# Performance work log

Hardware: AMD Instinct MI355X
Metric: run time of the kernel (lower is better)

Reference implementation:

```python
import jax, jax.numpy as jnp
import numpy as np

N_NODES = 50000
N_EDGES = 800000
D = 128        # in_channels == out_channels
EDGE_DIM = 32
EPS = 0.0      # GINEConv default eps


def setup_inputs() -> dict:
    key = jax.random.key(0)
    ks = jax.random.split(key, 12)
    s = lambda d: 1.0 / np.sqrt(d)
    inp = {
        "x": jax.random.normal(ks[0], (N_NODES, D), jnp.float32),
        "edge_index": jax.random.randint(ks[1], (2, N_EDGES), 0, N_NODES, jnp.int64),
        "edge_attr": jax.random.normal(ks[2], (N_EDGES, EDGE_DIM), jnp.float32),
        "importance": jax.random.uniform(ks[3], (N_NODES, 1), jnp.float32),
        # GINEConv edge lin: Linear(edge_dim, in_channels)
        "We": jax.random.uniform(ks[4], (EDGE_DIM, D), jnp.float32, -s(EDGE_DIM), s(EDGE_DIM)),
        "be": jax.random.uniform(ks[5], (D,), jnp.float32, -s(EDGE_DIM), s(EDGE_DIM)),
        # GINEConv nn: Linear(in_channels, out_channels)
        "Wc": jax.random.uniform(ks[6], (D, D), jnp.float32, -s(D), s(D)),
        "bc": jax.random.uniform(ks[7], (D,), jnp.float32, -s(D), s(D)),
        # importance_gate: Linear(out_channels + 1, out_channels)
        "Wg": jax.random.uniform(ks[8], (D + 1, D), jnp.float32, -s(D + 1), s(D + 1)),
        "bg": jax.random.uniform(ks[9], (D,), jnp.float32, -s(D + 1), s(D + 1)),
        # importance_propagation: Linear(out_channels, 1)
        "Wp": jax.random.uniform(ks[10], (D, 1), jnp.float32, -s(D), s(D)),
        "bp": jax.random.uniform(ks[11], (1,), jnp.float32, -s(D), s(D)),
    }
    return inp


def reference(x, edge_index, edge_attr, importance, We, be, Wc, bc, Wg, bg, Wp, bp):
    src, dst = edge_index[0], edge_index[1]
    # GINEConv: messages = relu(x_j + lin(edge_attr)), aggregated by sum at dst
    e = edge_attr @ We + be                      # [E, D]
    msg = jax.nn.relu(x[src] + e)                # [E, D] gather + fused add/relu
    agg = jax.ops.segment_sum(msg, dst, num_segments=N_NODES)  # [N, D] scatter-add
    conv_out = ((1.0 + EPS) * x + agg) @ Wc + bc  # [N, D]
    # importance gating + residual
    gate_in = jnp.concatenate([conv_out, importance], axis=-1)  # [N, D+1]
    gate = jax.nn.sigmoid(gate_in @ Wg + bg)
    out = gate * conv_out + (1.0 - gate) * x
    propagated_importance = out @ Wp + bp        # [N, 1]
    return (out, propagated_importance)
```

## Files before the change

kernel.cpp:

```cpp
#include <hip/hip_runtime.h>

#define NN 50000
#define NE 800000
#define DD 128
#define ED 32
#define NB 196

typedef short  bf16x8 __attribute__((ext_vector_type(8)));
typedef float  f32x4  __attribute__((ext_vector_type(4)));
typedef float  f32x16 __attribute__((ext_vector_type(16)));

__device__ __forceinline__ float4 ld4(const float* p) {
    return *reinterpret_cast<const float4*>(p);
}
__device__ __forceinline__ short f2bf(float f) {
    unsigned u = __float_as_uint(f);
    u += 0x7fffu + ((u >> 16) & 1u);
    return (short)(u >> 16);
}
__device__ __forceinline__ int sniff64(const int* ei) {
    return ((ei[1] | ei[3] | ei[5] | ei[7]) == 0) ? 1 : 0;
}

__global__ __launch_bounds__(256)
void k_setup(const float* __restrict__ x, const int* __restrict__ ei,
             const float* __restrict__ We, unsigned int* __restrict__ xb,
             int* __restrict__ counts, unsigned short* __restrict__ Bft)
{
    const int tid = threadIdx.x;
    if (blockIdx.x < 6250) {
        const int t = blockIdx.x * 256 + tid;
        if (t >= NN * 32) return;
        const int n = t >> 5, c = t & 31;
        const float* xr = x + (size_t)n * DD + c;
        const unsigned b0 = (unsigned short)f2bf(xr[0]);
        const unsigned b1 = (unsigned short)f2bf(xr[32]);
        const unsigned b2 = (unsigned short)f2bf(xr[64]);
        const unsigned b3 = (unsigned short)f2bf(xr[96]);
        xb[(size_t)n * 64 + c * 2]     = b0 | (b1 << 16);
        xb[(size_t)n * 64 + c * 2 + 1] = b2 | (b3 << 16);
    } else if (blockIdx.x < 8298) {
        const int is64 = sniff64(ei);
        const int2* ei2 = (const int2*)ei;
        for (int e = (blockIdx.x - 6250) * 256 + tid; e < NE; e += 2048 * 256) {
            const int dst = is64 ? ei2[NE + e].x : ei[NE + e];
            atomicAdd(&counts[dst], 1);
        }
    } else if (tid < 64) {
        const int col = tid & 31, h = tid >> 5;
#pragma unroll
        for (int bb = 0; bb < 4; ++bb)
#pragma unroll
            for (int s = 0; s < 2; ++s)
#pragma unroll
                for (int i = 0; i < 8; ++i)
                    Bft[tid * 64 + (bb * 2 + s) * 8 + i] =
                        (unsigned short)f2bf(We[(s * 16 + h * 8 + i) * DD + bb * 32 + col]);
    }
}

__global__ __launch_bounds__(256)
void k_bsum(const int* __restrict__ counts, int* __restrict__ bsum) {
    const int i = blockIdx.x * 256 + threadIdx.x;
    int c = (i < NN) ? counts[i] : 0;
#pragma unroll
    for (int off = 32; off; off >>= 1) c += __shfl_xor(c, off, 64);
    __shared__ int ws4[4];
    if ((threadIdx.x & 63) == 0) ws4[threadIdx.x >> 6] = c;
    __syncthreads();
    if (threadIdx.x == 0) bsum[blockIdx.x] = ws4[0] + ws4[1] + ws4[2] + ws4[3];
}

__global__ __launch_bounds__(256)
void k_scanb(const int* __restrict__ bsum, int* __restrict__ bexcl) {
    const int tid = threadIdx.x, lane = tid & 63, w = tid >> 6;
    const int v = (tid < NB) ? bsum[tid] : 0;
    int s = v;
#pragma unroll
    for (int off = 1; off < 64; off <<= 1) {
        const int t = __shfl_up(s, off, 64);
        if (lane >= off) s += t;
    }
    __shared__ int wsum[4], wexcl[4];
    if (lane == 63) wsum[w] = s;
    __syncthreads();
    if (tid == 0) {
        int r = 0;
#pragma unroll
        for (int k = 0; k < 4; ++k) { wexcl[k] = r; r += wsum[k]; }
    }
    __syncthreads();
    if (tid < NB) bexcl[tid] = wexcl[w] + s - v;
}

__global__ __launch_bounds__(256)
void k_rowptr(const int* __restrict__ counts, const int* __restrict__ bexcl,
              int* __restrict__ cursor) {
    const int tid = threadIdx.x, lane = tid & 63, w = tid >> 6;
    const int i = blockIdx.x * 256 + tid;
    const int c = (i < NN) ? counts[i] : 0;
    int s = c;
#pragma unroll
    for (int off = 1; off < 64; off <<= 1) {
        const int t = __shfl_up(s, off, 64);
        if (lane >= off) s += t;
    }
    __shared__ int wsum[4], wexcl[4];
    if (lane == 63) wsum[w] = s;
    __syncthreads();
    if (tid == 0) {
        int r = 0;
#pragma unroll
        for (int k = 0; k < 4; ++k) { wexcl[k] = r; r += wsum[k]; }
    }
    __syncthreads();
    if (i < NN) cursor[i] = bexcl[blockIdx.x] + wexcl[w] + s - c;
}

__global__ __launch_bounds__(256)
void k_scatter2(const int* __restrict__ ei, int* __restrict__ cursor,
                const float* __restrict__ ea, int2* __restrict__ sdat,
                unsigned int* __restrict__ eb)
{
    const int tid = threadIdx.x;
    const int e0  = blockIdx.x * 128;
    if (tid < 128) {
        const int is64 = sniff64(ei);
        const int2* ei2 = (const int2*)ei;
        const int e   = e0 + tid;
        const int src = is64 ? ei2[e].x : ei[e];
        const int dst = is64 ? ei2[NE + e].x : ei[NE + e];
        const int pos = atomicAdd(&cursor[dst], 1);
        sdat[pos] = make_int2(src | (dst << 16), e);
    }
#pragma unroll
    for (int it = 0; it < 8; ++it) {
        const int idx = it * 256 + tid;
        const float2 v = *reinterpret_cast<const float2*>(
                             ea + (size_t)e0 * ED + idx * 2);
        const unsigned lo = (unsigned short)f2bf(v.x);
        const unsigned hi = (unsigned short)f2bf(v.y);
        eb[(size_t)e0 * 16 + idx] = lo | (hi << 16);
    }
}

__device__ __forceinline__ void agg_epilogue(f32x16 (&C)[4], const float beb[4],
                                             int dstv, int lane, int col, int h,
                                             float* __restrict__ agg)
{
#pragma unroll
    for (int bb = 0; bb < 4; ++bb)
#pragma unroll
        for (int reg = 0; reg < 16; ++reg)
            C[bb][reg] = fmaxf(C[bb][reg] + beb[bb], 0.0f);

    const int  prv  = __shfl(dstv, (lane == 0) ? 0 : lane - 1, 64);
    const bool flag = (lane < 32) && ((col == 0) || (dstv != prv));
    unsigned rem = (unsigned)(__ballot(flag) & 0xFFFFFFFFull);

    while (rem) {
        const int ms = __ffs((int)rem) - 1;
        rem &= rem - 1;
        const int hi = rem ? (__ffs((int)rem) - 1) : 32;
        const int d  = __shfl(dstv, ms, 64);

        float v0 = 0.f, v1 = 0.f, v2 = 0.f, v3 = 0.f;
#pragma unroll
        for (int reg = 0; reg < 16; ++reg) {
            const int E = (reg & 3) + 8 * (reg >> 2) + 4 * h;
            const float mk = (E >= ms && E < hi) ? 1.0f : 0.0f;
            v0 = fmaf(mk, C[0][reg], v0);
            v1 = fmaf(mk, C[1][reg], v1);
            v2 = fmaf(mk, C[2][reg], v2);
            v3 = fmaf(mk, C[3][reg], v3);
        }
        v0 += __shfl_xor(v0, 32, 64);
        v1 += __shfl_xor(v1, 32, 64);
        v2 += __shfl_xor(v2, 32, 64);
        v3 += __shfl_xor(v3, 32, 64);

        float* ar = agg + (size_t)d * DD + h * 64 + col;
        unsafeAtomicAdd(ar,      h ? v2 : v0);
        unsafeAtomicAdd(ar + 32, h ? v3 : v1);
    }
}

__global__ __launch_bounds__(256, 2)
void k_aggE(const unsigned int* __restrict__ xb, const unsigned int* __restrict__ eb,
            const unsigned short* __restrict__ Bft, const float* __restrict__ be,
            const int2* __restrict__ sdat, float* __restrict__ agg)
{
    const int lane = threadIdx.x & 63;
    const int col  = lane & 31;
    const int h    = lane >> 5;
    const int wid  = (blockIdx.x << 2) | (threadIdx.x >> 6);
    const int c0   = wid * 2, c1 = wid * 2 + 1;

    bf16x8 Bf[4][2];
    {
        const bf16x8* bp_ = reinterpret_cast<const bf16x8*>(Bft + lane * 64);
#pragma unroll
        for (int bb = 0; bb < 4; ++bb) {
            Bf[bb][0] = bp_[bb * 2];
            Bf[bb][1] = bp_[bb * 2 + 1];
        }
    }
    float beb[4];
#pragma unroll
    for (int bb = 0; bb < 4; ++bb) beb[bb] = be[bb * 32 + col];

    const int2 dv0 = sdat[(size_t)c0 * 32 + col];
    const int2 dv1 = sdat[(size_t)c1 * 32 + col];

    const unsigned int* ebr0 = eb + (size_t)dv0.y * 16;
    const unsigned int* ebr1 = eb + (size_t)dv1.y * 16;
    const bf16x8 A00 = *reinterpret_cast<const bf16x8*>(ebr0 + h * 4);
    const bf16x8 A01 = *reinterpret_cast<const bf16x8*>(ebr0 + 8 + h * 4);
    const bf16x8 A10 = *reinterpret_cast<const bf16x8*>(ebr1 + h * 4);
    const bf16x8 A11 = *reinterpret_cast<const bf16x8*>(ebr1 + 8 + h * 4);

    uint2 w0[16];
#pragma unroll
    for (int reg = 0; reg < 16; ++reg) {
        const int E   = (reg & 3) + 8 * (reg >> 2) + 4 * h;
        const int src = __shfl(dv0.x, E, 64) & 0xFFFF;
        w0[reg] = *reinterpret_cast<const uint2*>(xb + (size_t)src * 64 + col * 2);
    }

    f32x16 C[4];
#pragma unroll
    for (int reg = 0; reg < 16; ++reg) {
        C[0][reg] = __uint_as_float(w0[reg].x << 16);
        C[1][reg] = __uint_as_float(w0[reg].x & 0xFFFF0000u);
        C[2][reg] = __uint_as_float(w0[reg].y << 16);
        C[3][reg] = __uint_as_float(w0[reg].y & 0xFFFF0000u);
    }
#pragma unroll
    for (int bb = 0; bb < 4; ++bb) {
        C[bb] = __builtin_amdgcn_mfma_f32_32x32x16_bf16(A00, Bf[bb][0], C[bb], 0, 0, 0);
        C[bb] = __builtin_amdgcn_mfma_f32_32x32x16_bf16(A01, Bf[bb][1], C[bb], 0, 0, 0);
    }

    uint2 w1[16];
#pragma unroll
    for (int reg = 0; reg < 16; ++reg) {
        const int E   = (reg & 3) + 8 * (reg >> 2) + 4 * h;
        const int src = __shfl(dv1.x, E, 64) & 0xFFFF;
        w1[reg] = *reinterpret_cast<const uint2*>(xb + (size_t)src * 64 + col * 2);
    }

    agg_epilogue(C, beb, ((unsigned)dv0.x) >> 16, lane, col, h, agg);

#pragma unroll
    for (int reg = 0; reg < 16; ++reg) {
        C[0][reg] = __uint_as_float(w1[reg].x << 16);
        C[1][reg] = __uint_as_float(w1[reg].x & 0xFFFF0000u);
        C[2][reg] = __uint_as_float(w1[reg].y << 16);
        C[3][reg] = __uint_as_float(w1[reg].y & 0xFFFF0000u);
    }
#pragma unroll
    for (int bb = 0; bb < 4; ++bb) {
        C[bb] = __builtin_amdgcn_mfma_f32_32x32x16_bf16(A10, Bf[bb][0], C[bb], 0, 0, 0);
        C[bb] = __builtin_amdgcn_mfma_f32_32x32x16_bf16(A11, Bf[bb][1], C[bb], 0, 0, 0);
    }
    agg_epilogue(C, beb, ((unsigned)dv1.x) >> 16, lane, col, h, agg);
}

__global__ __launch_bounds__(256)
void k_cg(const float* __restrict__ x, const float* agg,
          const float* __restrict__ Wc, const float* __restrict__ bc,
          const float* __restrict__ imp, const float* __restrict__ Wg,
          const float* __restrict__ bg, const float* __restrict__ Wp,
          const float* __restrict__ bp, float* outp, float* __restrict__ prop)
{
    __shared__ short sBh[2048 * 8];
    __shared__ short sBl[2048 * 8];
    for (int idx = threadIdx.x; idx < 2048; idx += 256) {
        const int kk = idx >> 9;
        const int b  = (idx >> 6) & 7;
        const int l  = idx & 63;
        const int row0 = kk * 32 + ((l >> 4) << 3);
        const int col  = b * 16 + (l & 15);
        bf16x8 h8;
#pragma unroll
        for (int j = 0; j < 8; ++j)
            h8[j] = f2bf(Wc[(row0 + j) * DD + col]);
        *reinterpret_cast<bf16x8*>(&sBh[idx * 8]) = h8;
    }
    __syncthreads();

    const int lane = threadIdx.x & 63;
    const int ncol = lane & 15;
    const int krow = (lane >> 4) << 3;
    const int grp  = lane >> 4;
    const int wib  = threadIdx.x >> 6;
    const int wid  = (blockIdx.x << 2) | wib;
    const bool live = (wid < NN / 16);
    const int m0 = live ? wid * 16 : 0;

    f32x4 C[8];
#pragma unroll
    for (int b = 0; b < 8; ++b) {
        const float bcv = bc[b * 16 + ncol];
        f32x4 c = { bcv, bcv, bcv, bcv };
        C[b] = c;
    }
    {
        const float* xrow = x   + (size_t)(m0 + ncol) * DD + krow;
        const float* grow = agg + (size_t)(m0 + ncol) * DD + krow;
#pragma unroll
        for (int kk = 0; kk < 4; ++kk) {
            const float4 x0 = ld4(xrow + kk * 32), x1 = ld4(xrow + kk * 32 + 4);
            const float4 g0 = ld4(grow + kk * 32), g1 = ld4(grow + kk * 32 + 4);
            const float av[8] = { x0.x + g0.x, x0.y + g0.y, x0.z + g0.z, x0.w + g0.w,
                                  x1.x + g1.x, x1.y + g1.y, x1.z + g1.z, x1.w + g1.w };
            bf16x8 Ah;
#pragma unroll
            for (int j = 0; j < 8; ++j) Ah[j] = f2bf(av[j]);
#pragma unroll
            for (int b = 0; b < 8; ++b) {
                const bf16x8 Bh = *reinterpret_cast<const bf16x8*>(&sBh[((kk * 8 + b) * 64 + lane) * 8]);
                C[b] = __builtin_amdgcn_mfma_f32_16x16x32_bf16(Ah, Bh, C[b], 0, 0, 0);
            }
        }
    }
    __syncthreads();

    for (int idx = threadIdx.x; idx < 2048; idx += 256) {
        const int kk = idx >> 9;
        const int b  = (idx >> 6) & 7;
        const int l  = idx & 63;
        const int row0 = kk * 32 + ((l >> 4) << 3);
        const int col  = b * 16 + (l & 15);
        bf16x8 h8;
#pragma unroll
        for (int j = 0; j < 8; ++j)
            h8[j] = f2bf(Wg[(row0 + j) * DD + col]);
        *reinterpret_cast<bf16x8*>(&sBh[idx * 8]) = h8;
    }
    float* scr = reinterpret_cast<float*>(sBl) + wib * 2048;
#pragma unroll
    for (int r = 0; r < 4; ++r)
#pragma unroll
        for (int b = 0; b < 8; ++b)
            scr[(grp * 4 + r) * DD + b * 16 + ncol] = C[b][r];
    __syncthreads();

    f32x4 Z[8];
#pragma unroll
    for (int b = 0; b < 8; ++b) {
        const float bgv = bg[b * 16 + ncol];
        f32x4 z = { bgv, bgv, bgv, bgv };
        Z[b] = z;
    }
#pragma unroll
    for (int kk = 0; kk < 4; ++kk) {
        const float4 a0 = ld4(scr + ncol * DD + kk * 32 + krow);
        const float4 a1 = ld4(scr + ncol * DD + kk * 32 + krow + 4);
        const float av[8] = { a0.x, a0.y, a0.z, a0.w, a1.x, a1.y, a1.z, a1.w };
        bf16x8 Ah;
#pragma unroll
        for (int j = 0; j < 8; ++j) Ah[j] = f2bf(av[j]);
#pragma unroll
        for (int b = 0; b < 8; ++b) {
            const bf16x8 Bh = *reinterpret_cast<const bf16x8*>(&sBh[((kk * 8 + b) * 64 + lane) * 8]);
            Z[b] = __builtin_amdgcn_mfma_f32_16x16x32_bf16(Ah, Bh, Z[b], 0, 0, 0);
        }
    }

    if (!live) return;

    float wgi[8], wp8[8];
#pragma unroll
    for (int b = 0; b < 8; ++b) {
        wgi[b] = Wg[DD * DD + b * 16 + ncol];
        wp8[b] = Wp[b * 16 + ncol];
    }
    const float bps = bp[0];

    float s[4] = { 0.f, 0.f, 0.f, 0.f };
#pragma unroll
    for (int r = 0; r < 4; ++r) {
        const int m = m0 + grp * 4 + r;
        const float im = imp[m];
        const float* xr = x + (size_t)m * DD + ncol;
        float* orow = outp + (size_t)m * DD + ncol;
#pragma unroll
        for (int b = 0; b < 8; ++b) {
            const float a = Z[b][r] + im * wgi[b];
            const float g = 1.0f / (1.0f + expf(-a));
            const float xv = xr[b * 16];
            const float o = fmaf(g, C[b][r] - xv, xv);
            orow[b * 16] = o;
            s[r] += o * wp8[b];
        }
    }
#pragma unroll
    for (int off = 1; off < 16; off <<= 1) {
        s[0] += __shfl_xor(s[0], off, 64);
        s[1] += __shfl_xor(s[1], off, 64);
        s[2] += __shfl_xor(s[2], off, 64);
        s[3] += __shfl_xor(s[3], off, 64);
    }
    if (ncol < 4) {
        const float v = (ncol == 0) ? s[0] : (ncol == 1) ? s[1] : (ncol == 2) ? s[2] : s[3];
        prop[m0 + grp * 4 + ncol] = v + bps;
    }
}

extern "C" void kernel_launch(void* const* d_in, const int* in_sizes, int n_in,
                              void* d_out, int out_size, void* d_ws, size_t ws_size,
                              hipStream_t stream) {
    const float* x   = (const float*)d_in[0];
    const int*   ei  = (const int*)d_in[1];
    const float* ea  = (const float*)d_in[2];
    const float* imp = (const float*)d_in[3];
    const float* We  = (const float*)d_in[4];
    const float* be  = (const float*)d_in[5];
    const float* Wc  = (const float*)d_in[6];
    const float* bc  = (const float*)d_in[7];
    const float* Wg  = (const float*)d_in[8];
    const float* bg  = (const float*)d_in[9];
    const float* Wp  = (const float*)d_in[10];
    const float* bp  = (const float*)d_in[11];

    float* out  = (float*)d_out;
    float* prop = out + (size_t)NN * DD;
    float* agg  = out;

    int*            counts = (int*)d_ws;
    int*            cursor = (int*)((char*)d_ws + 204800);
    int*            bsum   = (int*)((char*)d_ws + 409600);
    int*            bexcl  = (int*)((char*)d_ws + 413696);
    unsigned short* Bft    = (unsigned short*)((char*)d_ws + 417792);
    int2*           sdat   = (int2*)((char*)d_ws + 1048576);
    unsigned int*   xb     = (unsigned int*)((char*)d_ws + 7448576);
    unsigned int*   eb     = (unsigned int*)((char*)d_ws + 20248576);

    hipMemsetAsync(counts, 0, NN * sizeof(int), stream);
    hipMemsetAsync(agg, 0, (size_t)NN * DD * sizeof(float), stream);
    hipLaunchKernelGGL(k_setup,    dim3(8299), dim3(256), 0, stream,
                       x, ei, We, xb, counts, Bft);
    hipLaunchKernelGGL(k_bsum,     dim3(NB),   dim3(256), 0, stream, counts, bsum);
    hipLaunchKernelGGL(k_scanb,    dim3(1),    dim3(256), 0, stream, bsum, bexcl);
    hipLaunchKernelGGL(k_rowptr,   dim3(NB),   dim3(256), 0, stream, counts, bexcl, cursor);
    hipLaunchKernelGGL(k_scatter2, dim3(6250), dim3(256), 0, stream,
                       ei, cursor, ea, sdat, eb);
    hipLaunchKernelGGL(k_aggE,     dim3(3125), dim3(256), 0, stream,
                       xb, eb, Bft, be, sdat, agg);
    hipLaunchKernelGGL(k_cg,       dim3(782),  dim3(256), 0, stream,
                       x, agg, Wc, bc, imp, Wg, bg, Wp, bp, out, prop);
}
```

Measured before the change: 201.7 us.

## Switch edge aggregation to 16x16x32 MFMA tiles with 16 edges per wave

Reworks the edge-message kernel to use 16x16x32 bf16 MFMA, so each wave handles 16 edges instead of two 32-edge chunks. The bf16 copy of x is re-laid out so each lane fetches 8 contiguous bf16 values (16 bytes) per gathered source row. Occupancy is raised to 4 blocks per CU and the grid grows to 12500 blocks to hide gather latency. Segments are smaller, so runs of the same destination are split more often, which means more atomic adds per destination, and each wave does less work per launch.

```diff
diff --git a/kernel.cpp b/kernel.cpp
--- a/kernel.cpp
+++ b/kernel.cpp
@@ -8,7 +8,6 @@
 
 typedef short  bf16x8 __attribute__((ext_vector_type(8)));
 typedef float  f32x4  __attribute__((ext_vector_type(4)));
-typedef float  f32x16 __attribute__((ext_vector_type(16)));
 
 __device__ __forceinline__ float4 ld4(const float* p) {
     return *reinterpret_cast<const float4*>(p);
@@ -24,38 +23,34 @@
 
 __global__ __launch_bounds__(256)
 void k_setup(const float* __restrict__ x, const int* __restrict__ ei,
-             const float* __restrict__ We, unsigned int* __restrict__ xb,
+             const float* __restrict__ We, unsigned short* __restrict__ xb16,
              int* __restrict__ counts, unsigned short* __restrict__ Bft)
 {
     const int tid = threadIdx.x;
-    if (blockIdx.x < 6250) {
+    if (blockIdx.x < 3125) {
         const int t = blockIdx.x * 256 + tid;
-        if (t >= NN * 32) return;
-        const int n = t >> 5, c = t & 31;
+        if (t >= NN * 16) return;
+        const int n = t >> 4, c = t & 15;
         const float* xr = x + (size_t)n * DD + c;
-        const unsigned b0 = (unsigned short)f2bf(xr[0]);
-        const unsigned b1 = (unsigned short)f2bf(xr[32]);
-        const unsigned b2 = (unsigned short)f2bf(xr[64]);
-        const unsigned b3 = (unsigned short)f2bf(xr[96]);
-        xb[(size_t)n * 64 + c * 2]     = b0 | (b1 << 16);
-        xb[(size_t)n * 64 + c * 2 + 1] = b2 | (b3 << 16);
-    } else if (blockIdx.x < 8298) {
+        bf16x8 o;
+#pragma unroll
+        for (int bb = 0; bb < 8; ++bb) o[bb] = f2bf(xr[bb * 16]);
+        *reinterpret_cast<bf16x8*>(xb16 + (size_t)n * DD + c * 8) = o;
+    } else if (blockIdx.x < 5173) {
         const int is64 = sniff64(ei);
         const int2* ei2 = (const int2*)ei;
-        for (int e = (blockIdx.x - 6250) * 256 + tid; e < NE; e += 2048 * 256) {
+        for (int e = (blockIdx.x - 3125) * 256 + tid; e < NE; e += 2048 * 256) {
             const int dst = is64 ? ei2[NE + e].x : ei[NE + e];
             atomicAdd(&counts[dst], 1);
         }
     } else if (tid < 64) {
-        const int col = tid & 31, h = tid >> 5;
-#pragma unroll
-        for (int bb = 0; bb < 4; ++bb)
-#pragma unroll
-            for (int s = 0; s < 2; ++s)
-#pragma unroll
-                for (int i = 0; i < 8; ++i)
-                    Bft[tid * 64 + (bb * 2 + s) * 8 + i] =
-                        (unsigned short)f2bf(We[(s * 16 + h * 8 + i) * DD + bb * 32 + col]);
+        const int ncol = tid & 15, grp = tid >> 4;
+#pragma unroll
+        for (int bb = 0; bb < 8; ++bb)
+#pragma unroll
+            for (int i = 0; i < 8; ++i)
+                Bft[tid * 64 + bb * 8 + i] =
+                    (unsigned short)f2bf(We[(grp * 8 + i) * DD + bb * 16 + ncol]);
     }
 }
 
@@ -144,126 +139,80 @@
     }
 }
 
-__device__ __forceinline__ void agg_epilogue(f32x16 (&C)[4], const float beb[4],
-                                             int dstv, int lane, int col, int h,
-                                             float* __restrict__ agg)
-{
-#pragma unroll
-    for (int bb = 0; bb < 4; ++bb)
-#pragma unroll
-        for (int reg = 0; reg < 16; ++reg)
-            C[bb][reg] = fmaxf(C[bb][reg] + beb[bb], 0.0f);
-
-    const int  prv  = __shfl(dstv, (lane == 0) ? 0 : lane - 1, 64);
-    const bool flag = (lane < 32) && ((col == 0) || (dstv != prv));
-    unsigned rem = (unsigned)(__ballot(flag) & 0xFFFFFFFFull);
-
-    while (rem) {
-        const int ms = __ffs((int)rem) - 1;
-        rem &= rem - 1;
-        const int hi = rem ? (__ffs((int)rem) - 1) : 32;
-        const int d  = __shfl(dstv, ms, 64);
-
-        float v0 = 0.f, v1 = 0.f, v2 = 0.f, v3 = 0.f;
-#pragma unroll
-        for (int reg = 0; reg < 16; ++reg) {
-            const int E = (reg & 3) + 8 * (reg >> 2) + 4 * h;
-            const float mk = (E >= ms && E < hi) ? 1.0f : 0.0f;
-            v0 = fmaf(mk, C[0][reg], v0);
-            v1 = fmaf(mk, C[1][reg], v1);
-            v2 = fmaf(mk, C[2][reg], v2);
-            v3 = fmaf(mk, C[3][reg], v3);
-        }
-        v0 += __shfl_xor(v0, 32, 64);
-        v1 += __shfl_xor(v1, 32, 64);
-        v2 += __shfl_xor(v2, 32, 64);
-        v3 += __shfl_xor(v3, 32, 64);
-
-        float* ar = agg + (size_t)d * DD + h * 64 + col;
-        unsafeAtomicAdd(ar,      h ? v2 : v0);
-        unsafeAtomicAdd(ar + 32, h ? v3 : v1);
-    }
-}
-
-__global__ __launch_bounds__(256, 2)
-void k_aggE(const unsigned int* __restrict__ xb, const unsigned int* __restrict__ eb,
+__global__ __launch_bounds__(256, 4)
+void k_aggE(const unsigned short* __restrict__ xb16, const unsigned int* __restrict__ eb,
             const unsigned short* __restrict__ Bft, const float* __restrict__ be,
             const int2* __restrict__ sdat, float* __restrict__ agg)
 {
     const int lane = threadIdx.x & 63;
-    const int col  = lane & 31;
-    const int h    = lane >> 5;
+    const int ncol = lane & 15;
+    const int grp  = lane >> 4;
     const int wid  = (blockIdx.x << 2) | (threadIdx.x >> 6);
-    const int c0   = wid * 2, c1 = wid * 2 + 1;
-
-    bf16x8 Bf[4][2];
+
+    bf16x8 Bf[8];
     {
         const bf16x8* bp_ = reinterpret_cast<const bf16x8*>(Bft + lane * 64);
 #pragma unroll
-        for (int bb = 0; bb < 4; ++bb) {
-            Bf[bb][0] = bp_[bb * 2];
-            Bf[bb][1] = bp_[bb * 2 + 1];
+        for (int bb = 0; bb < 8; ++bb) Bf[bb] = bp_[bb];
+    }
+    float beb[8];
+#pragma unroll
+    for (int bb = 0; bb < 8; ++bb) beb[bb] = be[bb * 16 + ncol];
+
+    const int2 dv = sdat[(size_t)wid * 16 + ncol];
+
+    const bf16x8 Af = *reinterpret_cast<const bf16x8*>(
+                          eb + (size_t)dv.y * 16 + grp * 4);
+
+    f32x4 C[8];
+#pragma unroll
+    for (int r = 0; r < 4; ++r) {
+        const int srcm = __shfl(dv.x, (grp << 2) + r, 64) & 0xFFFF;
+        const bf16x8 w = *reinterpret_cast<const bf16x8*>(
+                             xb16 + (size_t)srcm * DD + ncol * 8);
+#pragma unroll
+        for (int bb = 0; bb < 8; ++bb)
+            C[bb][r] = __uint_as_float((unsigned)(unsigned short)w[bb] << 16);
+    }
+
+#pragma unroll
+    for (int bb = 0; bb < 8; ++bb)
+        C[bb] = __builtin_amdgcn_mfma_f32_16x16x32_bf16(Af, Bf[bb], C[bb], 0, 0, 0);
+
+#pragma unroll
+    for (int bb = 0; bb < 8; ++bb)
+#pragma unroll
+        for (int r = 0; r < 4; ++r)
+            C[bb][r] = fmaxf(C[bb][r] + beb[bb], 0.0f);
+
+    const int  dstv = ((unsigned)dv.x) >> 16;
+    const int  prv  = __shfl(dstv, (lane == 0) ? 0 : lane - 1, 64);
+    const bool flag = (lane < 16) && ((ncol == 0) || (dstv != prv));
+    unsigned rem = (unsigned)(__ballot(flag) & 0xFFFFu);
+
+    while (rem) {
+        const int ms = __ffs((int)rem) - 1;
+        rem &= rem - 1;
+        const int hi = rem ? (__ffs((int)rem) - 1) : 16;
+        const int d  = __shfl(dstv, ms, 64);
+
+        float red[8];
+#pragma unroll
+        for (int bb = 0; bb < 8; ++bb) {
+            float t = 0.0f;
+#pragma unroll
+            for (int r = 0; r < 4; ++r) {
+                const int m = (grp << 2) + r;
+                t = fmaf((m >= ms && m < hi) ? 1.0f : 0.0f, C[bb][r], t);
+            }
+            t += __shfl_xor(t, 16, 64);
+            t += __shfl_xor(t, 32, 64);
+            red[bb] = t;
         }
-    }
-    float beb[4];
-#pragma unroll
-    for (int bb = 0; bb < 4; ++bb) beb[bb] = be[bb * 32 + col];
-
-    const int2 dv0 = sdat[(size_t)c0 * 32 + col];
-    const int2 dv1 = sdat[(size_t)c1 * 32 + col];
-
-    const unsigned int* ebr0 = eb + (size_t)dv0.y * 16;
-    const unsigned int* ebr1 = eb + (size_t)dv1.y * 16;
-    const bf16x8 A00 = *reinterpret_cast<const bf16x8*>(ebr0 + h * 4);
-    const bf16x8 A01 = *reinterpret_cast<const bf16x8*>(ebr0 + 8 + h * 4);
-    const bf16x8 A10 = *reinterpret_cast<const bf16x8*>(ebr1 + h * 4);
-    const bf16x8 A11 = *reinterpret_cast<const bf16x8*>(ebr1 + 8 + h * 4);
-
-    uint2 w0[16];
-#pragma unroll
-    for (int reg = 0; reg < 16; ++reg) {
-        const int E   = (reg & 3) + 8 * (reg >> 2) + 4 * h;
-        const int src = __shfl(dv0.x, E, 64) & 0xFFFF;
-        w0[reg] = *reinterpret_cast<const uint2*>(xb + (size_t)src * 64 + col * 2);
-    }
-
-    f32x16 C[4];
-#pragma unroll
-    for (int reg = 0; reg < 16; ++reg) {
-        C[0][reg] = __uint_as_float(w0[reg].x << 16);
-        C[1][reg] = __uint_as_float(w0[reg].x & 0xFFFF0000u);
-        C[2][reg] = __uint_as_float(w0[reg].y << 16);
-        C[3][reg] = __uint_as_float(w0[reg].y & 0xFFFF0000u);
-    }
-#pragma unroll
-    for (int bb = 0; bb < 4; ++bb) {
-        C[bb] = __builtin_amdgcn_mfma_f32_32x32x16_bf16(A00, Bf[bb][0], C[bb], 0, 0, 0);
-        C[bb] = __builtin_amdgcn_mfma_f32_32x32x16_bf16(A01, Bf[bb][1], C[bb], 0, 0, 0);
-    }
-
-    uint2 w1[16];
-#pragma unroll
-    for (int reg = 0; reg < 16; ++reg) {
-        const int E   = (reg & 3) + 8 * (reg >> 2) + 4 * h;
-        const int src = __shfl(dv1.x, E, 64) & 0xFFFF;
-        w1[reg] = *reinterpret_cast<const uint2*>(xb + (size_t)src * 64 + col * 2);
-    }
-
-    agg_epilogue(C, beb, ((unsigned)dv0.x) >> 16, lane, col, h, agg);
-
-#pragma unroll
-    for (int reg = 0; reg < 16; ++reg) {
-        C[0][reg] = __uint_as_float(w1[reg].x << 16);
-        C[1][reg] = __uint_as_float(w1[reg].x & 0xFFFF0000u);
-        C[2][reg] = __uint_as_float(w1[reg].y << 16);
-        C[3][reg] = __uint_as_float(w1[reg].y & 0xFFFF0000u);
-    }
-#pragma unroll
-    for (int bb = 0; bb < 4; ++bb) {
-        C[bb] = __builtin_amdgcn_mfma_f32_32x32x16_bf16(A10, Bf[bb][0], C[bb], 0, 0, 0);
-        C[bb] = __builtin_amdgcn_mfma_f32_32x32x16_bf16(A11, Bf[bb][1], C[bb], 0, 0, 0);
-    }
-    agg_epilogue(C, beb, ((unsigned)dv1.x) >> 16, lane, col, h, agg);
+        float* ar = agg + (size_t)d * DD + (grp << 1) * 16 + ncol;
+        unsafeAtomicAdd(ar,      (grp == 0) ? red[0] : (grp == 1) ? red[2] : (grp == 2) ? red[4] : red[6]);
+        unsafeAtomicAdd(ar + 16, (grp == 0) ? red[1] : (grp == 1) ? red[3] : (grp == 2) ? red[5] : red[7]);
+    }
 }
 
 __global__ __launch_bounds__(256)
@@ -434,20 +383,20 @@
     int*            bexcl  = (int*)((char*)d_ws + 413696);
     unsigned short* Bft    = (unsigned short*)((char*)d_ws + 417792);
     int2*           sdat   = (int2*)((char*)d_ws + 1048576);
-    unsigned int*   xb     = (unsigned int*)((char*)d_ws + 7448576);
+    unsigned short* xb16   = (unsigned short*)((char*)d_ws + 7448576);
     unsigned int*   eb     = (unsigned int*)((char*)d_ws + 20248576);
 
     hipMemsetAsync(counts, 0, NN * sizeof(int), stream);
     hipMemsetAsync(agg, 0, (size_t)NN * DD * sizeof(float), stream);
-    hipLaunchKernelGGL(k_setup,    dim3(8299), dim3(256), 0, stream,
-                       x, ei, We, xb, counts, Bft);
-    hipLaunchKernelGGL(k_bsum,     dim3(NB),   dim3(256), 0, stream, counts, bsum);
-    hipLaunchKernelGGL(k_scanb,    dim3(1),    dim3(256), 0, stream, bsum, bexcl);
-    hipLaunchKernelGGL(k_rowptr,   dim3(NB),   dim3(256), 0, stream, counts, bexcl, cursor);
-    hipLaunchKernelGGL(k_scatter2, dim3(6250), dim3(256), 0, stream,
+    hipLaunchKernelGGL(k_setup,    dim3(5174),  dim3(256), 0, stream,
+                       x, ei, We, xb16, counts, Bft);
+    hipLaunchKernelGGL(k_bsum,     dim3(NB),    dim3(256), 0, stream, counts, bsum);
+    hipLaunchKernelGGL(k_scanb,    dim3(1),     dim3(256), 0, stream, bsum, bexcl);
+    hipLaunchKernelGGL(k_rowptr,   dim3(NB),    dim3(256), 0, stream, counts, bexcl, cursor);
+    hipLaunchKernelGGL(k_scatter2, dim3(6250),  dim3(256), 0, stream,
                        ei, cursor, ea, sdat, eb);
-    hipLaunchKernelGGL(k_aggE,     dim3(3125), dim3(256), 0, stream,
-                       xb, eb, Bft, be, sdat, agg);
-    hipLaunchKernelGGL(k_cg,       dim3(782),  dim3(256), 0, stream,
+    hipLaunchKernelGGL(k_aggE,     dim3(12500), dim3(256), 0, stream,
+                       xb16, eb, Bft, be, sdat, agg);
+    hipLaunchKernelGGL(k_cg,       dim3(782),   dim3(256), 0, stream,
                        x, agg, Wc, bc, imp, Wg, bg, Wp, bp, out, prop);
 }
```

New measurement: 208.6 us. +3.4%, slower.
